# Performance work log

Measured on AMD Instinct MI355X. Metric: run time of the kernel, lower is better.

The kernel has to match this reference:

```python
import jax, jax.numpy as jnp
import numpy as np

NUM_CORR = 256  # uniform per-item k (init arg num_correspondences = [256]*8)


def setup_inputs() -> dict:
    key = jax.random.key(0)
    k1, k2, k3, k4 = jax.random.split(key, 4)
    B, N, M, D = 8, 2048, 2048, 256
    return {
        "ref_feats": jax.random.normal(k1, (N, D), dtype=jnp.float32),
        "src_feats": jax.random.normal(k2, (M, D), dtype=jnp.float32),
        "c_matrix": jax.random.uniform(k3, (B, N, M), dtype=jnp.float32),
        "gt_node_corr_indices": jax.random.randint(k4, (1000, 2), 0, N, dtype=jnp.int64) if jax.config.jax_enable_x64 else jax.random.randint(k4, (1000, 2), 0, N, dtype=jnp.int32),
    }


def reference(ref_feats, src_feats, c_matrix, gt_node_corr_indices):
    B, N, M = c_matrix.shape
    # Dual normalization: row-normalized * column-normalized scores.
    ref_scores = c_matrix / c_matrix.sum(axis=2, keepdims=True)  # [B,N,M]
    src_scores = c_matrix / c_matrix.sum(axis=1, keepdims=True)  # [B,N,M]
    scores = ref_scores * src_scores
    # Per-item flatten + top-k over all N*M entries.
    top_scores, top_idx = jax.lax.top_k(scores.reshape(B, N * M), NUM_CORR)  # [B,K]
    flat_idx = top_idx.reshape(-1)  # concatenation in batch order, as original loop
    # Default masks are all-True, so ref_indices/src_indices are identity arange.
    ref_corr_indices = flat_idx // M
    src_corr_indices = flat_idx % M
    corr_scores = top_scores.reshape(-1)
    return ref_corr_indices, src_corr_indices, corr_scores
```

## Files before the change

kernel.cpp:

```cpp
#include <hip/hip_runtime.h>
#include <stdint.h>

#define BB 8
#define NN 2048
#define MM 2048
#define KK 256
#define NMTOT (NN*MM)
#define NBIN 8192
#define CANDCAP 4096

typedef unsigned int u32;
typedef unsigned long long u64;

__device__ inline double dshflxor(double x, int m) {
  long long v = __double_as_longlong(x);
  int lo = (int)(v & 0xffffffffLL);
  int hi = (int)(v >> 32);
  lo = __shfl_xor(lo, m, 64);
  hi = __shfl_xor(hi, m, 64);
  return __longlong_as_double(((long long)hi << 32) | (u64)(u32)lo);
}

template <int RCROWS>
__global__ __launch_bounds__(256) void k_sums(const float* __restrict__ c,
                                              float* __restrict__ rs,
                                              double* __restrict__ cp) {
  int rc = blockIdx.x;
  int b  = blockIdx.y;
  int t = threadIdx.x;
  int wave = t >> 6, lane = t & 63;
  const int NCH = NN / RCROWS;
  const float* base = c + ((size_t)b * NN + (size_t)rc * RCROWS) * MM;
  double ca[8] = {0, 0, 0, 0, 0, 0, 0, 0};
  __shared__ double rowpart[RCROWS][4];
  #pragma unroll 2
  for (int r = 0; r < RCROWS; ++r) {
    const float4* row4 = (const float4*)(base + (size_t)r * MM);
    float4 a = row4[t];
    float4 bq = row4[t + 256];
    ca[0] += (double)a.x;  ca[1] += (double)a.y;
    ca[2] += (double)a.z;  ca[3] += (double)a.w;
    ca[4] += (double)bq.x; ca[5] += (double)bq.y;
    ca[6] += (double)bq.z; ca[7] += (double)bq.w;
    double rp = (double)a.x + (double)a.y + (double)a.z + (double)a.w
              + (double)bq.x + (double)bq.y + (double)bq.z + (double)bq.w;
    #pragma unroll
    for (int m2 = 32; m2 > 0; m2 >>= 1) rp += dshflxor(rp, m2);
    if (lane == 0) rowpart[r][wave] = rp;
  }
  __syncthreads();
  if (t < RCROWS) {
    double s = rowpart[t][0] + rowpart[t][1] + rowpart[t][2] + rowpart[t][3];
    rs[b * NN + rc * RCROWS + t] = (float)s;
  }
  double* cpb = cp + ((size_t)(b * NCH + rc)) * MM;
  *(double4*)(cpb + 4 * t)        = make_double4(ca[0], ca[1], ca[2], ca[3]);
  *(double4*)(cpb + 1024 + 4 * t) = make_double4(ca[4], ca[5], ca[6], ca[7]);
}

__global__ __launch_bounds__(256) void k_colsum(const double* __restrict__ cp,
                                                float* __restrict__ cs, int nch) {
  int idx = blockIdx.x * 256 + threadIdx.x;
  int b = idx >> 11;
  int col = idx & (MM - 1);
  double acc = 0.0;
  for (int q = 0; q < nch; ++q) acc += cp[(size_t)(b * nch + q) * MM + col];
  cs[idx] = (float)acc;
}

__global__ __launch_bounds__(256) void k_hist(const float* __restrict__ c, const float* __restrict__ rs,
                                              const float* __restrict__ cs, u32* __restrict__ ghist) {
  __shared__ u32 h[NBIN];
  for (int i = threadIdx.x; i < NBIN; i += 256) h[i] = 0;
  __syncthreads();
  int b = blockIdx.x >> 6;
  int blk = blockIdx.x & 63;
  const float4* cb = (const float4*)(c + (size_t)b * NMTOT);
  const float* rsb = rs + b * NN;
  const float* csb = cs + b * MM;
  int base = blk * 16384;
  for (int it = 0; it < 64; ++it) {
    int v4 = base + it * 256 + threadIdx.x;
    float4 v = cb[v4];
    int fe = v4 << 2;
    int n = fe >> 11;
    int m = fe & (MM - 1);
    float rv = rsb[n];
    float s0 = (v.x / rv) * (v.x / csb[m]);
    float s1 = (v.y / rv) * (v.y / csb[m + 1]);
    float s2 = (v.z / rv) * (v.z / csb[m + 2]);
    float s3 = (v.w / rv) * (v.w / csb[m + 3]);
    atomicAdd(&h[__float_as_uint(s0) >> 18], 1u);
    atomicAdd(&h[__float_as_uint(s1) >> 18], 1u);
    atomicAdd(&h[__float_as_uint(s2) >> 18], 1u);
    atomicAdd(&h[__float_as_uint(s3) >> 18], 1u);
  }
  __syncthreads();
  u32* gh = ghist + b * NBIN;
  for (int i = threadIdx.x; i < NBIN; i += 256) {
    u32 x = h[i];
    if (x) atomicAdd(&gh[i], x);
  }
}

__global__ __launch_bounds__(256) void k_thresh(const u32* __restrict__ ghist, u32* __restrict__ T) {
  __shared__ u32 lsum[256];
  int b = blockIdx.x;
  const u32* gh = ghist + b * NBIN;
  int t = threadIdx.x;
  u32 s = 0;
  for (int k = 0; k < 32; ++k) s += gh[NBIN - 1 - (t * 32 + k)];
  lsum[t] = s;
  __syncthreads();
  if (t == 0) {
    u32 cum = 0; u32 thr = 0; bool found = false;
    for (int q = 0; q < 256 && !found; ++q) {
      if (cum + lsum[q] >= KK) {
        u32 c2 = cum;
        for (int k = 0; k < 32; ++k) {
          int bin = NBIN - 1 - (q * 32 + k);
          c2 += gh[bin];
          if (c2 >= KK) { thr = (u32)bin; found = true; break; }
        }
      } else {
        cum += lsum[q];
      }
    }
    T[b] = thr;
  }
}

__global__ __launch_bounds__(256) void k_collect(const float* __restrict__ c, const float* __restrict__ rs,
                                                 const float* __restrict__ cs, const u32* __restrict__ T,
                                                 u32* __restrict__ cnt, u64* __restrict__ cand) {
  int b = blockIdx.x >> 6;
  int blk = blockIdx.x & 63;
  const float4* cb = (const float4*)(c + (size_t)b * NMTOT);
  const float* rsb = rs + b * NN;
  const float* csb = cs + b * MM;
  u32 thr = T[b];
  u64* cd = cand + (size_t)b * CANDCAP;
  int base = blk * 16384;
  for (int it = 0; it < 64; ++it) {
    int v4 = base + it * 256 + threadIdx.x;
    float4 v = cb[v4];
    int fe = v4 << 2;
    int n = fe >> 11;
    int m = fe & (MM - 1);
    float rv = rsb[n];
    float s[4];
    s[0] = (v.x / rv) * (v.x / csb[m]);
    s[1] = (v.y / rv) * (v.y / csb[m + 1]);
    s[2] = (v.z / rv) * (v.z / csb[m + 2]);
    s[3] = (v.w / rv) * (v.w / csb[m + 3]);
    #pragma unroll
    for (int j = 0; j < 4; ++j) {
      u32 bits = __float_as_uint(s[j]);
      if ((bits >> 18) >= thr) {
        u32 pos = atomicAdd(&cnt[b], 1u);
        if (pos < CANDCAP) {
          u64 key = ((u64)bits << 32) | (u64)(0xFFFFFFFFu - (u32)(fe + j));
          cd[pos] = key;
        }
      }
    }
  }
}

__global__ __launch_bounds__(256) void k_sort(const u32* __restrict__ cnt, const u64* __restrict__ cand,
                                              float* __restrict__ out) {
  __shared__ u64 keys[CANDCAP];
  int b = blockIdx.x;
  u32 n = cnt[b]; if (n > CANDCAP) n = CANDCAP;
  int size = 512;
  while (size < (int)n) size <<= 1;
  const u64* cd = cand + (size_t)b * CANDCAP;
  for (int i = threadIdx.x; i < size; i += 256)
    keys[i] = (i < (int)n) ? cd[i] : 0ull;
  for (int ssize = 2; ssize <= size; ssize <<= 1) {
    for (int stride = ssize >> 1; stride > 0; stride >>= 1) {
      __syncthreads();
      for (int k = threadIdx.x; k < size; k += 256) {
        int p = k ^ stride;
        if (p > k) {
          u64 a = keys[k], bb2 = keys[p];
          bool up = ((k & ssize) == 0);
          bool sw = up ? (a < bb2) : (a > bb2);
          if (sw) { keys[k] = bb2; keys[p] = a; }
        }
      }
    }
  }
  __syncthreads();
  int k = threadIdx.x;
  if (k < KK) {
    u64 key = keys[k];
    u32 idx = 0xFFFFFFFFu - (u32)(key & 0xFFFFFFFFull);
    float sc = __uint_as_float((u32)(key >> 32));
    out[b * KK + k]                 = (float)(idx >> 11);
    out[BB * KK + b * KK + k]       = (float)(idx & (MM - 1));
    out[2 * BB * KK + b * KK + k]   = sc;
  }
}

extern "C" void kernel_launch(void* const* d_in, const int* in_sizes, int n_in,
                              void* d_out, int out_size, void* d_ws, size_t ws_size,
                              hipStream_t stream) {
  const float* c = (const float*)d_in[2];
  char* ws = (char*)d_ws;
  float* out = (float*)d_out;

  const size_t cp32 = (size_t)BB * 64 * MM * 8;
  const size_t cp64 = (size_t)BB * 32 * MM * 8;
  bool use32 = ws_size >= (131072 + cp32 + NBIN * BB * 4 + 512 + (size_t)BB * CANDCAP * 8);
  size_t cpBytes = use32 ? cp32 : cp64;
  int nch = use32 ? 64 : 32;

  float*  rs    = (float*)(ws);
  float*  cs    = (float*)(ws + 65536);
  double* cp    = (double*)(ws + 131072);
  u32*    ghist = (u32*)(ws + 131072 + cpBytes);
  u32*    cnt   = (u32*)(ws + 131072 + cpBytes + NBIN * BB * 4);
  u32*    T     = (u32*)(ws + 131072 + cpBytes + NBIN * BB * 4 + 256);
  u64*    cand  = (u64*)(ws + 131072 + cpBytes + NBIN * BB * 4 + 512);

  hipMemsetAsync(ghist, 0, NBIN * BB * 4 + 256, stream);

  if (use32) k_sums<32><<<dim3(64, 8), 256, 0, stream>>>(c, rs, cp);
  else       k_sums<64><<<dim3(32, 8), 256, 0, stream>>>(c, rs, cp);
  k_colsum <<<64, 256, 0, stream>>>(cp, cs, nch);
  k_hist   <<<512, 256, 0, stream>>>(c, rs, cs, ghist);
  k_thresh <<<8, 256, 0, stream>>>(ghist, T);
  k_collect<<<512, 256, 0, stream>>>(c, rs, cs, T, cnt, cand);
  k_sort   <<<8, 256, 0, stream>>>(cnt, cand, out);
}
```

Baseline: 381.1 us.

## Use reciprocal multiplies in scan passes and recompute exact scores in sort

```diff
diff --git a/kernel.cpp b/kernel.cpp
--- a/kernel.cpp
+++ b/kernel.cpp
@@ -7,7 +7,7 @@
 #define KK 256
 #define NMTOT (NN*MM)
 #define NBIN 8192
-#define CANDCAP 4096
+#define CANDCAP 8192
 
 typedef unsigned int u32;
 typedef unsigned long long u64;
@@ -59,37 +59,45 @@
 }
 
 __global__ __launch_bounds__(256) void k_colsum(const double* __restrict__ cp,
-                                                float* __restrict__ cs, int nch) {
+                                                const float* __restrict__ rs,
+                                                float* __restrict__ cs,
+                                                float* __restrict__ rrs,
+                                                float* __restrict__ rcs, int nch) {
   int idx = blockIdx.x * 256 + threadIdx.x;
   int b = idx >> 11;
   int col = idx & (MM - 1);
   double acc = 0.0;
   for (int q = 0; q < nch; ++q) acc += cp[(size_t)(b * nch + q) * MM + col];
-  cs[idx] = (float)acc;
-}
-
-__global__ __launch_bounds__(256) void k_hist(const float* __restrict__ c, const float* __restrict__ rs,
-                                              const float* __restrict__ cs, u32* __restrict__ ghist) {
+  float csv = (float)acc;
+  cs[idx] = csv;
+  rcs[idx] = 1.0f / csv;
+  rrs[idx] = 1.0f / rs[idx];
+}
+
+__global__ __launch_bounds__(256) void k_hist(const float* __restrict__ c,
+                                              const float* __restrict__ rrs,
+                                              const float* __restrict__ rcs,
+                                              u32* __restrict__ ghist) {
   __shared__ u32 h[NBIN];
   for (int i = threadIdx.x; i < NBIN; i += 256) h[i] = 0;
   __syncthreads();
-  int b = blockIdx.x >> 6;
-  int blk = blockIdx.x & 63;
+  int b = blockIdx.x >> 7;
+  int blk = blockIdx.x & 127;
   const float4* cb = (const float4*)(c + (size_t)b * NMTOT);
-  const float* rsb = rs + b * NN;
-  const float* csb = cs + b * MM;
-  int base = blk * 16384;
-  for (int it = 0; it < 64; ++it) {
+  const float* rsb = rrs + b * NN;
+  const float* csb = rcs + b * MM;
+  int base = blk * 8192;
+  for (int it = 0; it < 32; ++it) {
     int v4 = base + it * 256 + threadIdx.x;
     float4 v = cb[v4];
     int fe = v4 << 2;
     int n = fe >> 11;
     int m = fe & (MM - 1);
     float rv = rsb[n];
-    float s0 = (v.x / rv) * (v.x / csb[m]);
-    float s1 = (v.y / rv) * (v.y / csb[m + 1]);
-    float s2 = (v.z / rv) * (v.z / csb[m + 2]);
-    float s3 = (v.w / rv) * (v.w / csb[m + 3]);
+    float s0 = (v.x * rv) * (v.x * csb[m]);
+    float s1 = (v.y * rv) * (v.y * csb[m + 1]);
+    float s2 = (v.z * rv) * (v.z * csb[m + 2]);
+    float s3 = (v.w * rv) * (v.w * csb[m + 3]);
     atomicAdd(&h[__float_as_uint(s0) >> 18], 1u);
     atomicAdd(&h[__float_as_uint(s1) >> 18], 1u);
     atomicAdd(&h[__float_as_uint(s2) >> 18], 1u);
@@ -130,18 +138,20 @@
   }
 }
 
-__global__ __launch_bounds__(256) void k_collect(const float* __restrict__ c, const float* __restrict__ rs,
-                                                 const float* __restrict__ cs, const u32* __restrict__ T,
-                                                 u32* __restrict__ cnt, u64* __restrict__ cand) {
-  int b = blockIdx.x >> 6;
-  int blk = blockIdx.x & 63;
+__global__ __launch_bounds__(256) void k_collect(const float* __restrict__ c,
+                                                 const float* __restrict__ rrs,
+                                                 const float* __restrict__ rcs,
+                                                 const u32* __restrict__ T,
+                                                 u32* __restrict__ cnt, u32* __restrict__ cand) {
+  int b = blockIdx.x >> 7;
+  int blk = blockIdx.x & 127;
   const float4* cb = (const float4*)(c + (size_t)b * NMTOT);
-  const float* rsb = rs + b * NN;
-  const float* csb = cs + b * MM;
+  const float* rsb = rrs + b * NN;
+  const float* csb = rcs + b * MM;
   u32 thr = T[b];
-  u64* cd = cand + (size_t)b * CANDCAP;
-  int base = blk * 16384;
-  for (int it = 0; it < 64; ++it) {
+  u32* cd = cand + (size_t)b * CANDCAP;
+  int base = blk * 8192;
+  for (int it = 0; it < 32; ++it) {
     int v4 = base + it * 256 + threadIdx.x;
     float4 v = cb[v4];
     int fe = v4 << 2;
@@ -149,34 +159,45 @@
     int m = fe & (MM - 1);
     float rv = rsb[n];
     float s[4];
-    s[0] = (v.x / rv) * (v.x / csb[m]);
-    s[1] = (v.y / rv) * (v.y / csb[m + 1]);
-    s[2] = (v.z / rv) * (v.z / csb[m + 2]);
-    s[3] = (v.w / rv) * (v.w / csb[m + 3]);
+    s[0] = (v.x * rv) * (v.x * csb[m]);
+    s[1] = (v.y * rv) * (v.y * csb[m + 1]);
+    s[2] = (v.z * rv) * (v.z * csb[m + 2]);
+    s[3] = (v.w * rv) * (v.w * csb[m + 3]);
     #pragma unroll
     for (int j = 0; j < 4; ++j) {
       u32 bits = __float_as_uint(s[j]);
-      if ((bits >> 18) >= thr) {
+      if (((bits + 16u) >> 18) >= thr) {
         u32 pos = atomicAdd(&cnt[b], 1u);
-        if (pos < CANDCAP) {
-          u64 key = ((u64)bits << 32) | (u64)(0xFFFFFFFFu - (u32)(fe + j));
-          cd[pos] = key;
-        }
+        if (pos < CANDCAP) cd[pos] = (u32)(fe + j);
       }
     }
   }
 }
 
-__global__ __launch_bounds__(256) void k_sort(const u32* __restrict__ cnt, const u64* __restrict__ cand,
+__global__ __launch_bounds__(256) void k_sort(const u32* __restrict__ cnt, const u32* __restrict__ cand,
+                                              const float* __restrict__ c,
+                                              const float* __restrict__ rs,
+                                              const float* __restrict__ cs,
                                               float* __restrict__ out) {
   __shared__ u64 keys[CANDCAP];
   int b = blockIdx.x;
   u32 n = cnt[b]; if (n > CANDCAP) n = CANDCAP;
   int size = 512;
   while (size < (int)n) size <<= 1;
-  const u64* cd = cand + (size_t)b * CANDCAP;
-  for (int i = threadIdx.x; i < size; i += 256)
-    keys[i] = (i < (int)n) ? cd[i] : 0ull;
+  const u32* cd = cand + (size_t)b * CANDCAP;
+  const float* cb = c + (size_t)b * NMTOT;
+  const float* rsb = rs + b * NN;
+  const float* csb = cs + b * MM;
+  for (int i = threadIdx.x; i < size; i += 256) {
+    u64 key = 0ull;
+    if (i < (int)n) {
+      u32 idx = cd[i];
+      float v = cb[idx];
+      float sc = (v / rsb[idx >> 11]) * (v / csb[idx & (MM - 1)]);
+      key = ((u64)__float_as_uint(sc) << 32) | (u64)(0xFFFFFFFFu - idx);
+    }
+    keys[i] = key;
+  }
   for (int ssize = 2; ssize <= size; ssize <<= 1) {
     for (int stride = ssize >> 1; stride > 0; stride >>= 1) {
       __syncthreads();
@@ -212,25 +233,29 @@
 
   const size_t cp32 = (size_t)BB * 64 * MM * 8;
   const size_t cp64 = (size_t)BB * 32 * MM * 8;
-  bool use32 = ws_size >= (131072 + cp32 + NBIN * BB * 4 + 512 + (size_t)BB * CANDCAP * 8);
+  const size_t fixedHead = 4 * 65536;
+  const size_t tail = (size_t)NBIN * BB * 4 + 512 + (size_t)BB * CANDCAP * 4;
+  bool use32 = ws_size >= (fixedHead + cp32 + tail);
   size_t cpBytes = use32 ? cp32 : cp64;
   int nch = use32 ? 64 : 32;
 
   float*  rs    = (float*)(ws);
   float*  cs    = (float*)(ws + 65536);
-  double* cp    = (double*)(ws + 131072);
-  u32*    ghist = (u32*)(ws + 131072 + cpBytes);
-  u32*    cnt   = (u32*)(ws + 131072 + cpBytes + NBIN * BB * 4);
-  u32*    T     = (u32*)(ws + 131072 + cpBytes + NBIN * BB * 4 + 256);
-  u64*    cand  = (u64*)(ws + 131072 + cpBytes + NBIN * BB * 4 + 512);
-
-  hipMemsetAsync(ghist, 0, NBIN * BB * 4 + 256, stream);
+  float*  rrs   = (float*)(ws + 131072);
+  float*  rcs   = (float*)(ws + 196608);
+  double* cp    = (double*)(ws + fixedHead);
+  u32*    ghist = (u32*)(ws + fixedHead + cpBytes);
+  u32*    cnt   = (u32*)(ws + fixedHead + cpBytes + (size_t)NBIN * BB * 4);
+  u32*    T     = (u32*)(ws + fixedHead + cpBytes + (size_t)NBIN * BB * 4 + 64);
+  u32*    cand  = (u32*)(ws + fixedHead + cpBytes + (size_t)NBIN * BB * 4 + 512);
+
+  hipMemsetAsync(ghist, 0, (size_t)NBIN * BB * 4 + 512, stream);
 
   if (use32) k_sums<32><<<dim3(64, 8), 256, 0, stream>>>(c, rs, cp);
   else       k_sums<64><<<dim3(32, 8), 256, 0, stream>>>(c, rs, cp);
-  k_colsum <<<64, 256, 0, stream>>>(cp, cs, nch);
-  k_hist   <<<512, 256, 0, stream>>>(c, rs, cs, ghist);
+  k_colsum <<<64, 256, 0, stream>>>(cp, rs, cs, rrs, rcs, nch);
+  k_hist   <<<1024, 256, 0, stream>>>(c, rrs, rcs, ghist);
   k_thresh <<<8, 256, 0, stream>>>(ghist, T);
-  k_collect<<<512, 256, 0, stream>>>(c, rs, cs, T, cnt, cand);
-  k_sort   <<<8, 256, 0, stream>>>(cnt, cand, out);
-}
+  k_collect<<<1024, 256, 0, stream>>>(c, rrs, rcs, T, cnt, cand);
+  k_sort   <<<8, 256, 0, stream>>>(cnt, cand, c, rs, cs, out);
+}
```

Measured after the change: 368.2 us. 3.4% less time.
